# Performance work log

Hardware: AMD Instinct MI355X
Metric: run time of the kernel (lower is better)

## Reference

```python
import jax, jax.numpy as jnp
import numpy as np

C = 256; G = 8; GC = C // G; K = 3; PAD = 1; DIL = 1; STRIDE = 1
P = K * K
BN_EPS = 1e-5; LN_EPS = 1e-5


def setup_inputs() -> dict:
    key = jax.random.key(0)
    ks = jax.random.split(key, 8)
    def rn(k, shape, scale=0.02):
        return jax.random.normal(k, shape, jnp.float32) * scale
    B, H, W = 8, 56, 56
    return dict(
        x=jax.random.normal(ks[0], (B, C, H, W), jnp.float32),
        w_in=rn(ks[1], (C, C)), b_in=jnp.zeros((C,), jnp.float32),
        dw_w=rn(ks[2], (C, 1, K, K)), dw_b=jnp.zeros((C,), jnp.float32),
        ln_g=jnp.ones((C,), jnp.float32), ln_b=jnp.zeros((C,), jnp.float32),
        w_off=rn(ks[3], (C, G * P * 2)), b_off=jnp.zeros((G * P * 2,), jnp.float32),
        w_mask=rn(ks[4], (C, G * P)), b_mask=jnp.zeros((G * P,), jnp.float32),
        w_out=rn(ks[5], (C, C)), b_out=jnp.zeros((C,), jnp.float32),
        bn_g=jnp.ones((C,), jnp.float32), bn_b=jnp.zeros((C,), jnp.float32),
        bn_mean=jnp.zeros((C,), jnp.float32),
        bn_var=jnp.ones((C,), jnp.float32),
    )


def _forward(x, w_in, b_in, dw_w, dw_b, ln_g, ln_b, w_off, b_off,
             w_mask, b_mask, w_out, b_out, bn_g, bn_b, bn_mean, bn_var):
    B, _, H, W = x.shape
    x_nhwc = jnp.transpose(x, (0, 2, 3, 1))                    # [B,H,W,C]
    v = x_nhwc @ w_in + b_in                                   # input_proj

    # offset/mask branch: depthwise conv (NCHW) + LayerNorm (channels_last) + GELU
    f = jax.lax.conv_general_dilated(
        x, dw_w, (1, 1), [(PAD, PAD), (PAD, PAD)],
        feature_group_count=C,
        dimension_numbers=('NCHW', 'OIHW', 'NCHW')) + dw_b[None, :, None, None]
    f = jnp.transpose(f, (0, 2, 3, 1))                         # [B,H,W,C]
    mu = f.mean(-1, keepdims=True)
    var = f.var(-1, keepdims=True)
    f = (f - mu) * jax.lax.rsqrt(var + LN_EPS) * ln_g + ln_b
    f = jax.nn.gelu(f, approximate=False)

    offset = (f @ w_off + b_off).reshape(B, H, W, G, P, 2)     # (x, y) pairs
    mask = jax.nn.softmax((f @ w_mask + b_mask).reshape(B, H, W, G, P), axis=-1)

    # zero-pad projected features (dcnv3_core_pytorch pads before sampling)
    vp = jnp.pad(v, ((0, 0), (PAD, PAD), (PAD, PAD), (0, 0)))
    Hin, Win = H + 2 * PAD, W + 2 * PAD

    # reference points + kernel dilation grid, normalized to padded extent
    base = (DIL * (K - 1)) // 2 + 0.5
    ref_y = (base + jnp.arange(H, dtype=jnp.float32) * STRIDE) / Hin   # [H]
    ref_x = (base + jnp.arange(W, dtype=jnp.float32) * STRIDE) / Win   # [W]
    kx = jnp.arange(K, dtype=jnp.float32) * DIL - (DIL * (K - 1)) // 2
    gx, gy = jnp.meshgrid(kx, kx, indexing='ij')               # torch meshgrid order
    grid_x = gx.reshape(-1) / Win                              # [P]
    grid_y = gy.reshape(-1) / Hin

    loc_x = ref_x[None, None, :, None, None] + grid_x[None, None, None, None, :] + offset[..., 0] / Win
    loc_y = ref_y[None, :, None, None, None] + grid_y[None, None, None, None, :] + offset[..., 1] / Hin
    # grid_sample(align_corners=False) pixel coords: p = loc * size - 0.5
    px = loc_x * Win - 0.5                                     # [B,H,W,G,P]
    py = loc_y * Hin - 0.5

    x0 = jnp.floor(px); y0 = jnp.floor(py)
    wx = px - x0; wy = py - y0
    x0i = x0.astype(jnp.int32); y0i = y0.astype(jnp.int32)
    x1i = x0i + 1; y1i = y0i + 1

    def valid(i, lim):
        return ((i >= 0) & (i < lim)).astype(v.dtype)
    vx0, vx1 = valid(x0i, Win), valid(x1i, Win)
    vy0, vy1 = valid(y0i, Hin), valid(y1i, Hin)
    x0c = jnp.clip(x0i, 0, Win - 1); x1c = jnp.clip(x1i, 0, Win - 1)
    y0c = jnp.clip(y0i, 0, Hin - 1); y1c = jnp.clip(y1i, 0, Hin - 1)

    vg = vp.reshape(B, Hin * Win, G, GC).transpose(0, 2, 1, 3).reshape(B * G, Hin * Win, GC)
    L = H * W

    def regroup(a):  # [B,H,W,G,P] -> [B*G, L*P]
        return a.reshape(B, L, G, P).transpose(0, 2, 1, 3).reshape(B * G, L * P)

    def gather(yc, xc):
        idx = regroup(yc * Win + xc)
        return jnp.take_along_axis(vg, idx[:, :, None], axis=1)   # [B*G, L*P, GC]

    sampled = (gather(y0c, x0c) * regroup((1 - wx) * (1 - wy) * vx0 * vy0)[:, :, None]
             + gather(y0c, x1c) * regroup(wx * (1 - wy) * vx1 * vy0)[:, :, None]
             + gather(y1c, x0c) * regroup((1 - wx) * wy * vx0 * vy1)[:, :, None]
             + gather(y1c, x1c) * regroup(wx * wy * vx1 * vy1)[:, :, None])

    m = mask.reshape(B, L, G, P).transpose(0, 2, 1, 3)             # [B,G,L,P]
    out = (sampled.reshape(B, G, L, P, GC) * m[..., None]).sum(3)  # [B,G,L,GC]
    out = out.transpose(0, 2, 1, 3).reshape(B, H, W, C)

    out = out @ w_out + b_out                                  # output_proj
    y = jnp.transpose(out, (0, 3, 1, 2))                       # NCHW
    y = (y - bn_mean[None, :, None, None]) * jax.lax.rsqrt(bn_var + BN_EPS)[None, :, None, None] \
        * bn_g[None, :, None, None] + bn_b[None, :, None, None]
    return y * jax.nn.sigmoid(y)                               # SiLU


def reference(x, w_in, b_in, dw_w, dw_b, ln_g, ln_b, w_off, b_off,
              w_mask, b_mask, w_out, b_out, bn_g, bn_b, bn_mean, bn_var):
    return _forward(x, w_in, b_in, dw_w, dw_b, ln_g, ln_b, w_off, b_off,
                    w_mask, b_mask, w_out, b_out, bn_g, bn_b, bn_mean, bn_var)
```

## Files before the change

kernel.cpp:

```cpp
#include <hip/hip_runtime.h>
#include <math.h>

#define BATCH 8
#define CH    256
#define HDIM  56
#define WDIM  56
#define HW    (HDIM*WDIM)
#define MTOT  (BATCH*HW)
#define GRP   8
#define GC    32
#define NP    9
#define NOFF  (GRP*NP*2)
#define NMSK  (GRP*NP)
#define NTOT  (NOFF+NMSK)
#define POSB  4
#define NBLK128 ((MTOT/128)*2)
#define NBLKOUT ((MTOT/64)*2)

typedef float f32x4 __attribute__((ext_vector_type(4)));
typedef short s16x8 __attribute__((ext_vector_type(8)));

__device__ inline void split2(float a, float b, unsigned int& hp, unsigned int& lp)
{
    const unsigned int ua = __float_as_uint(a), ub = __float_as_uint(b);
    hp = (ub & 0xffff0000u) | (ua >> 16);
    const float ha = __uint_as_float(ua & 0xffff0000u);
    const float hb = __uint_as_float(ub & 0xffff0000u);
    const unsigned int la = __float_as_uint(a - ha), lb = __float_as_uint(b - hb);
    lp = (lb & 0xffff0000u) | (la >> 16);
}

__device__ __forceinline__ void gld_lds16(const unsigned short* g, unsigned short* l)
{
    __builtin_amdgcn_global_load_lds(
        (const __attribute__((address_space(1))) unsigned int*)g,
        (__attribute__((address_space(3))) unsigned int*)l, 16, 0, 0);
}

__global__ __launch_bounds__(256)
void xt_split_kernel(const float* __restrict__ x,
                     unsigned short* __restrict__ hi,
                     unsigned short* __restrict__ lo)
{
    __shared__ float lds[64][68];
    const int hw0 = blockIdx.x * 64;
    const int k0  = blockIdx.y * 64;
    const int b   = blockIdx.z;
    const int t = threadIdx.x;
    #pragma unroll
    for (int p = 0; p < 4; ++p) {
        const int kr = (t >> 4) + p * 16;
        const int hc = (t & 15) * 4;
        *(float4*)&lds[kr][hc] =
            *(const float4*)(x + ((size_t)b * CH + k0 + kr) * HW + hw0 + hc);
    }
    __syncthreads();
    const int ml = t >> 2;
    const int kc = (t & 3) * 16;
    unsigned int hbuf[8], lbuf[8];
    #pragma unroll
    for (int j = 0; j < 16; j += 2)
        split2(lds[kc + j][ml], lds[kc + j + 1][ml], hbuf[j >> 1], lbuf[j >> 1]);
    const size_t row = (size_t)(b * HW + hw0 + ml) * CH + k0 + kc;
    *(uint4*)&hi[row]     = *(uint4*)&hbuf[0];
    *(uint4*)&hi[row + 8] = *(uint4*)&hbuf[4];
    *(uint4*)&lo[row]     = *(uint4*)&lbuf[0];
    *(uint4*)&lo[row + 8] = *(uint4*)&lbuf[4];
}

__device__ __forceinline__ void gemm128_body(
    const unsigned short* __restrict__ ahi,
    const unsigned short* __restrict__ alo,
    const unsigned short* __restrict__ whi,
    const unsigned short* __restrict__ wlo,
    unsigned short* sAh, unsigned short* sAl,
    unsigned short* sBh, unsigned short* sBl,
    int m0, int n0g, int t, f32x4 (&acc)[4][4])
{
    const int lane = t & 63, wv4 = t >> 6;
    const int wm = wv4 & 1, wn = wv4 >> 1;
    const int fm = lane & 15, q = lane >> 4;

    int srow[2], sgs[2], slb[2];
    #pragma unroll
    for (int i = 0; i < 2; ++i) {
        const int u = i * 256 + t;
        srow[i] = u >> 2;
        const int ss = u & 3;
        sgs[i] = ss ^ ((srow[i] >> 1) & 3);
        slb[i] = i * 2048 + wv4 * 512;
    }

    for (int kk = 0; kk < 8; ++kk) {
        const int k0 = kk * 32;
        #pragma unroll
        for (int i = 0; i < 2; ++i) {
            const size_t ga = (size_t)(m0 + srow[i]) * CH + k0 + sgs[i] * 8;
            const size_t gb = (size_t)(n0g + srow[i]) * CH + k0 + sgs[i] * 8;
            gld_lds16(ahi + ga, sAh + slb[i]);
            gld_lds16(alo + ga, sAl + slb[i]);
            gld_lds16(whi + gb, sBh + slb[i]);
            gld_lds16(wlo + gb, sBl + slb[i]);
        }
        __syncthreads();

        s16x8 ah[4], al[4], wh[4], wl[4];
        #pragma unroll
        for (int i = 0; i < 4; ++i) {
            const int ar = wm * 64 + i * 16 + fm;
            const int as = (q ^ ((ar >> 1) & 3)) * 8;
            ah[i] = *(const s16x8*)&sAh[ar * 32 + as];
            al[i] = *(const s16x8*)&sAl[ar * 32 + as];
            const int br = wn * 64 + i * 16 + fm;
            const int bs = (q ^ ((br >> 1) & 3)) * 8;
            wh[i] = *(const s16x8*)&sBh[br * 32 + bs];
            wl[i] = *(const s16x8*)&sBl[br * 32 + bs];
        }
        #pragma unroll
        for (int nt = 0; nt < 4; ++nt)
            #pragma unroll
            for (int mt = 0; mt < 4; ++mt) {
                acc[nt][mt] = __builtin_amdgcn_mfma_f32_16x16x32_bf16(wh[nt], ah[mt], acc[nt][mt], 0, 0, 0);
                acc[nt][mt] = __builtin_amdgcn_mfma_f32_16x16x32_bf16(wh[nt], al[mt], acc[nt][mt], 0, 0, 0);
                acc[nt][mt] = __builtin_amdgcn_mfma_f32_16x16x32_bf16(wl[nt], ah[mt], acc[nt][mt], 0, 0, 0);
            }
        __syncthreads();
    }
}

__global__ __launch_bounds__(256)
void gemm128_dual(const unsigned short* __restrict__ ahi1,
                  const unsigned short* __restrict__ alo1,
                  const unsigned short* __restrict__ whi1,
                  const unsigned short* __restrict__ wlo1,
                  const float* __restrict__ bias1,
                  float* __restrict__ out1,
                  const unsigned short* __restrict__ ahi2,
                  const unsigned short* __restrict__ alo2,
                  const unsigned short* __restrict__ whi2,
                  const unsigned short* __restrict__ wlo2,
                  const float* __restrict__ bias2,
                  float* __restrict__ out2)
{
    __shared__ unsigned short sAh[128*32], sAl[128*32], sBh[128*32], sBl[128*32];

    const int half = blockIdx.x >= NBLK128;
    const int lbid = blockIdx.x - (half ? NBLK128 : 0);
    const unsigned short* ahi = half ? ahi2 : ahi1;
    const unsigned short* alo = half ? alo2 : alo1;
    const unsigned short* whi = half ? whi2 : whi1;
    const unsigned short* wlo = half ? wlo2 : wlo1;
    const float* bias = half ? bias2 : bias1;
    float* out = half ? out2 : out1;

    const int sw = (lbid & 7) * (NBLK128 / 8) + (lbid >> 3);
    const int m0 = (sw >> 1) * 128;
    const int n0g = (sw & 1) * 128;
    const int t = threadIdx.x;
    const int lane = t & 63, wv4 = t >> 6;
    const int wm = wv4 & 1, wn = wv4 >> 1;
    const int fm = lane & 15, q = lane >> 4;

    f32x4 acc[4][4];
    const f32x4 zero = {0.0f, 0.0f, 0.0f, 0.0f};
    #pragma unroll
    for (int i = 0; i < 4; ++i)
        #pragma unroll
        for (int j = 0; j < 4; ++j) acc[i][j] = zero;

    gemm128_body(ahi, alo, whi, wlo, sAh, sAl, sBh, sBl, m0, n0g, t, acc);

    #pragma unroll
    for (int nt = 0; nt < 4; ++nt) {
        const int n = n0g + wn*64 + nt*16 + q*4;
        const float4 b4 = *(const float4*)&bias[n];
        #pragma unroll
        for (int mt = 0; mt < 4; ++mt) {
            const int mm = m0 + wm*64 + mt*16 + fm;
            f32x4 o = acc[nt][mt];
            o[0] += b4.x; o[1] += b4.y; o[2] += b4.z; o[3] += b4.w;
            *(f32x4*)&out[(size_t)mm * CH + n] = o;
        }
    }
}

__global__ __launch_bounds__(256)
void gemm_out_64x128(const unsigned short* __restrict__ ahi,
                     const unsigned short* __restrict__ alo,
                     const unsigned short* __restrict__ whi,
                     const unsigned short* __restrict__ wlo,
                     const float* __restrict__ bias,
                     const float* __restrict__ bn_g,
                     const float* __restrict__ bn_b,
                     const float* __restrict__ bn_mean,
                     const float* __restrict__ bn_var,
                     float* __restrict__ y)
{
    __shared__ unsigned short sAh[64*32], sAl[64*32], sBh[128*32], sBl[128*32];

    const int sw = (blockIdx.x & 7) * (NBLKOUT / 8) + (blockIdx.x >> 3);
    const int m0  = (sw >> 1) * 64;
    const int n0g = (sw & 1) * 128;
    const int t = threadIdx.x;
    const int lane = t & 63, wv4 = t >> 6;
    const int wm = wv4 >> 1, wn = wv4 & 1;
    const int fm = lane & 15, q = lane >> 4;

    f32x4 acc[4][2];
    const f32x4 zero = {0.0f, 0.0f, 0.0f, 0.0f};
    #pragma unroll
    for (int i = 0; i < 4; ++i)
        #pragma unroll
        for (int j = 0; j < 2; ++j) acc[i][j] = zero;

    const int arow0 = t >> 2;
    const int asl0  = (t & 3) ^ ((arow0 >> 1) & 3);
    const int albase0 = wv4 * 512;
    int brow[2], bsl[2], blbase[2];
    #pragma unroll
    for (int i = 0; i < 2; ++i) {
        const int u = i * 256 + t;
        brow[i] = u >> 2;
        bsl[i] = (u & 3) ^ ((brow[i] >> 1) & 3);
        blbase[i] = i * 2048 + wv4 * 512;
    }

    for (int kk = 0; kk < 8; ++kk) {
        const int k0 = kk * 32;
        {
            const size_t ga = (size_t)(m0 + arow0) * CH + k0 + asl0 * 8;
            gld_lds16(ahi + ga, sAh + albase0);
            gld_lds16(alo + ga, sAl + albase0);
        }
        #pragma unroll
        for (int i = 0; i < 2; ++i) {
            const size_t gb = (size_t)(n0g + brow[i]) * CH + k0 + bsl[i] * 8;
            gld_lds16(whi + gb, sBh + blbase[i]);
            gld_lds16(wlo + gb, sBl + blbase[i]);
        }
        __syncthreads();

        s16x8 ah[2], al[2], wh[4], wl[4];
        #pragma unroll
        for (int i = 0; i < 2; ++i) {
            const int ar = wm * 32 + i * 16 + fm;
            const int as = (q ^ ((ar >> 1) & 3)) * 8;
            ah[i] = *(const s16x8*)&sAh[ar * 32 + as];
            al[i] = *(const s16x8*)&sAl[ar * 32 + as];
        }
        #pragma unroll
        for (int i = 0; i < 4; ++i) {
            const int br = wn * 64 + i * 16 + fm;
            const int bs = (q ^ ((br >> 1) & 3)) * 8;
            wh[i] = *(const s16x8*)&sBh[br * 32 + bs];
            wl[i] = *(const s16x8*)&sBl[br * 32 + bs];
        }
        #pragma unroll
        for (int nt = 0; nt < 4; ++nt)
            #pragma unroll
            for (int mt = 0; mt < 2; ++mt) {
                acc[nt][mt] = __builtin_amdgcn_mfma_f32_16x16x32_bf16(wh[nt], ah[mt], acc[nt][mt], 0, 0, 0);
                acc[nt][mt] = __builtin_amdgcn_mfma_f32_16x16x32_bf16(wh[nt], al[mt], acc[nt][mt], 0, 0, 0);
                acc[nt][mt] = __builtin_amdgcn_mfma_f32_16x16x32_bf16(wl[nt], ah[mt], acc[nt][mt], 0, 0, 0);
            }
        __syncthreads();
    }

    #pragma unroll
    for (int nt = 0; nt < 4; ++nt) {
        #pragma unroll
        for (int r = 0; r < 4; ++r) {
            const int n = n0g + wn*64 + nt*16 + q*4 + r;
            const float sc = bn_g[n] * rsqrtf(bn_var[n] + 1e-5f);
            const float sb = bn_b[n] - bn_mean[n] * sc;
            const float bs = bias[n];
            #pragma unroll
            for (int mt = 0; mt < 2; ++mt) {
                const int mm = m0 + wm*32 + mt*16 + fm;
                const int bimg = mm / HW, hw = mm % HW;
                float val = (acc[nt][mt][r] + bs) * sc + sb;
                y[(size_t)bimg * CH * HW + (size_t)n * HW + hw] = val / (1.0f + expf(-val));
            }
        }
    }
}

__global__ __launch_bounds__(256)
void gemm_in_mfma(const unsigned short* __restrict__ xhi,
                  const unsigned short* __restrict__ xlo,
                  const unsigned short* __restrict__ whi,
                  const unsigned short* __restrict__ wlo,
                  const float* __restrict__ bias,
                  float* __restrict__ v)
{
    const int m0 = blockIdx.x * 256;
    const int n0 = blockIdx.y * 64;
    const int t = threadIdx.x;
    const int lane = t & 63, wv = t >> 6;
    const int mblk = m0 + wv * 64;
    const int fm = lane & 15;
    const int q  = lane >> 4;

    f32x4 acc[4][4];
    const f32x4 zero = {0.0f, 0.0f, 0.0f, 0.0f};
    #pragma unroll
    for (int i = 0; i < 4; ++i)
        #pragma unroll
        for (int j = 0; j < 4; ++j) acc[i][j] = zero;

    const unsigned short *xrh[4], *xrl[4], *wrh[4], *wrl[4];
    #pragma unroll
    for (int mt = 0; mt < 4; ++mt) {
        xrh[mt] = xhi + (size_t)(mblk + mt*16 + fm) * CH + q * 8;
        xrl[mt] = xlo + (size_t)(mblk + mt*16 + fm) * CH + q * 8;
    }
    #pragma unroll
    for (int nt = 0; nt < 4; ++nt) {
        wrh[nt] = whi + (size_t)(n0 + nt*16 + fm) * CH + q * 8;
        wrl[nt] = wlo + (size_t)(n0 + nt*16 + fm) * CH + q * 8;
    }

    for (int k0 = 0; k0 < CH; k0 += 32) {
        s16x8 wh[4], wl[4], ah[4], al[4];
        #pragma unroll
        for (int nt = 0; nt < 4; ++nt) {
            wh[nt] = *(const s16x8*)(wrh[nt] + k0);
            wl[nt] = *(const s16x8*)(wrl[nt] + k0);
        }
        #pragma unroll
        for (int mt = 0; mt < 4; ++mt) {
            ah[mt] = *(const s16x8*)(xrh[mt] + k0);
            al[mt] = *(const s16x8*)(xrl[mt] + k0);
        }
        #pragma unroll
        for (int nt = 0; nt < 4; ++nt)
            #pragma unroll
            for (int mt = 0; mt < 4; ++mt) {
                acc[nt][mt] = __builtin_amdgcn_mfma_f32_16x16x32_bf16(wh[nt], ah[mt], acc[nt][mt], 0, 0, 0);
                acc[nt][mt] = __builtin_amdgcn_mfma_f32_16x16x32_bf16(wh[nt], al[mt], acc[nt][mt], 0, 0, 0);
                acc[nt][mt] = __builtin_amdgcn_mfma_f32_16x16x32_bf16(wl[nt], ah[mt], acc[nt][mt], 0, 0, 0);
            }
    }

    #pragma unroll
    for (int nt = 0; nt < 4; ++nt) {
        const float4 b4 = *(const float4*)&bias[n0 + nt*16 + q*4];
        #pragma unroll
        for (int mt = 0; mt < 4; ++mt) {
            f32x4 o = acc[nt][mt];
            o[0] += b4.x; o[1] += b4.y; o[2] += b4.z; o[3] += b4.w;
            *(f32x4*)&v[(size_t)(mblk + mt*16 + fm) * CH + n0 + nt*16 + q*4] = o;
        }
    }
}

__global__ __launch_bounds__(256)
void dw_ln_gelu_nhwc_split(const unsigned short* __restrict__ xhi,
                           const unsigned short* __restrict__ xlo,
                           const float* __restrict__ dw_w,
                           const float* __restrict__ dw_b,
                           const float* __restrict__ ln_g,
                           const float* __restrict__ ln_b,
                           unsigned short* __restrict__ fh,
                           unsigned short* __restrict__ fl)
{
    __shared__ float wt[NP][CH];
    __shared__ float lbias[CH], lgam[CH], lbet[CH];

    const int t = threadIdx.x;
    {
        const float* wp = dw_w + t * NP;
        #pragma unroll
        for (int p = 0; p < NP; ++p) wt[p][t] = wp[p];
        lbias[t] = dw_b[t]; lgam[t] = ln_g[t]; lbet[t] = ln_b[t];
    }
    __syncthreads();

    const int nblk = MTOT / POSB;
    const int per  = nblk / 8;
    const int bid  = blockIdx.x;
    const int sw   = (bid & 7) * per + (bid >> 3);
    const int q    = t >> 6, lane = t & 63;
    const int n    = sw * POSB + q;
    const int b    = n / HW;
    const int hw   = n % HW;
    const int h    = hw / WDIM, w = hw % WDIM;
    const int c4   = lane * 4;
    const size_t base = (size_t)b * HW * CH + c4;

    float ax = 0.0f, ay = 0.0f, az = 0.0f, aw = 0.0f;
    #pragma unroll
    for (int p = 0; p < NP; ++p) {
        const int hh = h + p / 3 - 1;
        const int ww = w + p % 3 - 1;
        if ((unsigned)hh >= (unsigned)HDIM || (unsigned)ww >= (unsigned)WDIM)
            continue;
        const size_t idx = base + (size_t)(hh * WDIM + ww) * CH;
        const ushort4 uh = *(const ushort4*)(xhi + idx);
        const ushort4 ul = *(const ushort4*)(xlo + idx);
        const float4 wv = *(const float4*)&wt[p][c4];
        ax = fmaf(__uint_as_float((unsigned)uh.x << 16), wv.x,
             fmaf(__uint_as_float((unsigned)ul.x << 16), wv.x, ax));
        ay = fmaf(__uint_as_float((unsigned)uh.y << 16), wv.y,
             fmaf(__uint_as_float((unsigned)ul.y << 16), wv.y, ay));
        az = fmaf(__uint_as_float((unsigned)uh.z << 16), wv.z,
             fmaf(__uint_as_float((unsigned)ul.z << 16), wv.z, az));
        aw = fmaf(__uint_as_float((unsigned)uh.w << 16), wv.w,
             fmaf(__uint_as_float((unsigned)ul.w << 16), wv.w, aw));
    }
    {
        const float4 b4 = *(const float4*)&lbias[c4];
        ax += b4.x; ay += b4.y; az += b4.z; aw += b4.w;
    }

    float s1 = ax + ay + az + aw;
    float s2 = ax*ax + ay*ay + az*az + aw*aw;
    #pragma unroll
    for (int off = 32; off > 0; off >>= 1) {
        s1 += __shfl_xor(s1, off);
        s2 += __shfl_xor(s2, off);
    }
    const float mean = s1 * (1.0f / 256.0f);
    const float rstd = rsqrtf(s2 * (1.0f / 256.0f) - mean * mean + 1e-5f);

    const float4 g4 = *(const float4*)&lgam[c4];
    const float4 e4 = *(const float4*)&lbet[c4];
    const float x0 = (ax - mean) * rstd * g4.x + e4.x;
    const float x1 = (ay - mean) * rstd * g4.y + e4.y;
    const float x2 = (az - mean) * rstd * g4.z + e4.z;
    const float x3 = (aw - mean) * rstd * g4.w + e4.w;
    const float o0 = 0.5f * x0 * (1.0f + erff(x0 * 0.70710678118654752f));
    const float o1 = 0.5f * x1 * (1.0f + erff(x1 * 0.70710678118654752f));
    const float o2 = 0.5f * x2 * (1.0f + erff(x2 * 0.70710678118654752f));
    const float o3 = 0.5f * x3 * (1.0f + erff(x3 * 0.70710678118654752f));

    unsigned int hp0, lp0, hp1, lp1;
    split2(o0, o1, hp0, lp0);
    split2(o2, o3, hp1, lp1);
    *(uint2*)&fh[(size_t)n * CH + c4] = make_uint2(hp0, hp1);
    *(uint2*)&fl[(size_t)n * CH + c4] = make_uint2(lp0, lp1);
}

__global__ __launch_bounds__(256)
void wt_split_kernel(const float* __restrict__ w,
                     unsigned short* __restrict__ hi,
                     unsigned short* __restrict__ lo)
{
    __shared__ float lds[64][68];
    const int kt = blockIdx.x * 64, nt = blockIdx.y * 64;
    const int t = threadIdx.x;
    #pragma unroll
    for (int p = 0; p < 4; ++p) {
        const int kr = (t >> 4) + p * 16, nc = (t & 15) * 4;
        *(float4*)&lds[kr][nc] = *(const float4*)(w + (size_t)(kt + kr) * CH + nt + nc);
    }
    __syncthreads();
    const int nl = t >> 2, kc = (t & 3) * 16;
    #pragma unroll
    for (int j = 0; j < 16; j += 2) {
        const float f0 = lds[kc + j][nl], f1 = lds[kc + j + 1][nl];
        unsigned int hp, lp;
        split2(f0, f1, hp, lp);
        *(unsigned int*)&hi[(size_t)(nt + nl) * CH + kt + kc + j] = hp;
        *(unsigned int*)&lo[(size_t)(nt + nl) * CH + kt + kc + j] = lp;
    }
}

__global__ __launch_bounds__(256)
void wt2_split_kernel(const float* __restrict__ w_off,
                      const float* __restrict__ w_mask,
                      const float* __restrict__ b_off,
                      const float* __restrict__ b_mask,
                      unsigned short* __restrict__ hi,
                      unsigned short* __restrict__ lo,
                      float* __restrict__ bcat)
{
    const int n = threadIdx.x;
    if (blockIdx.x == 0) {
        bcat[n] = (n < NOFF) ? b_off[n] : ((n < NTOT) ? b_mask[n - NOFF] : 0.0f);
    }
    const int k0 = blockIdx.x * 16;
    #pragma unroll
    for (int j = 0; j < 16; j += 2) {
        const int k = k0 + j;
        float f0 = 0.0f, f1 = 0.0f;
        if (n < NOFF) {
            f0 = w_off[(size_t)k * NOFF + n];
            f1 = w_off[(size_t)(k + 1) * NOFF + n];
        } else if (n < NTOT) {
            f0 = w_mask[(size_t)k * NMSK + (n - NOFF)];
            f1 = w_mask[(size_t)(k + 1) * NMSK + (n - NOFF)];
        }
        unsigned int hp, lp;
        split2(f0, f1, hp, lp);
        *(unsigned int*)&hi[(size_t)n * CH + k] = hp;
        *(unsigned int*)&lo[(size_t)n * CH + k] = lp;
    }
}

__global__ __launch_bounds__(256)
void sample_kernel_omb_split(const float* __restrict__ v,
                             const float* __restrict__ omb,
                             unsigned short* __restrict__ sh,
                             unsigned short* __restrict__ sl)
{
    __shared__ alignas(16) float loff[POSB][NOFF];
    __shared__ alignas(16) float lmsk[POSB][NMSK];
    __shared__ alignas(16) float wtab[POSB][GRP*NP][4];
    __shared__ alignas(16) int   itab[POSB][GRP*NP][4];

    const int nblk = MTOT / POSB;
    const int per  = nblk / 8;
    const int bid  = blockIdx.x;
    const int sw   = (bid % 8) * per + (bid / 8);
    const int n0 = sw * POSB;
    const int t = threadIdx.x;

    if (t < POSB * (NOFF/4)) {
        const int q = t / (NOFF/4), r = t % (NOFF/4);
        *(float4*)&loff[q][r*4] = *(const float4*)&omb[(size_t)(n0+q)*CH + r*4];
    } else if (t < POSB * (NOFF/4) + POSB * (NMSK/4)) {
        const int u = t - POSB * (NOFF/4);
        const int q = u / (NMSK/4), r = u % (NMSK/4);
        *(float4*)&lmsk[q][r*4] = *(const float4*)&omb[(size_t)(n0+q)*CH + NOFF + r*4];
    }
    __syncthreads();

    if (t < POSB * GRP) {
        const int q = t >> 3, g = t & 7;
        float* mm = &lmsk[q][g * NP];
        float mx = -1e30f;
        #pragma unroll
        for (int p = 0; p < NP; ++p) mx = fmaxf(mx, mm[p]);
        float sum = 0.0f;
        #pragma unroll
        for (int p = 0; p < NP; ++p) { const float e = __expf(mm[p] - mx); mm[p] = e; sum += e; }
        const float inv = 1.0f / sum;
        #pragma unroll
        for (int p = 0; p < NP; ++p) mm[p] *= inv;
    }
    __syncthreads();

    for (int u = t; u < POSB * GRP * NP; u += 256) {
        const int q = u / (GRP*NP), j = u % (GRP*NP);
        const int g = j / NP, p = j % NP;
        const int n = n0 + q;
        const int hw = n % HW;
        const int h = hw / WDIM, w = hw % WDIM;
        const float ox = loff[q][g*18 + p*2 + 0];
        const float oy = loff[q][g*18 + p*2 + 1];
        const float m  = lmsk[q][g*NP + p];
        const float px = (float)(w + p/3) + ox;
        const float py = (float)(h + p%3) + oy;
        const float fx = floorf(px), fy = floorf(py);
        const float wx = px - fx, wy = py - fy;
        const int x0 = (int)fx, y0 = (int)fy;
        const int x1 = x0 + 1, y1 = y0 + 1;
        const float vx0 = (x0 >= 1 && x0 < 57) ? 1.0f : 0.0f;
        const float vx1 = (x1 >= 1 && x1 < 57) ? 1.0f : 0.0f;
        const float vy0 = (y0 >= 1 && y0 < 57) ? 1.0f : 0.0f;
        const float vy1 = (y1 >= 1 && y1 < 57) ? 1.0f : 0.0f;
        const int x0c = min(max(x0, 1), 56), x1c = min(max(x1, 1), 56);
        const int y0c = min(max(y0, 1), 56), y1c = min(max(y1, 1), 56);
        wtab[q][j][0] = m * (1.0f-wx) * (1.0f-wy) * vx0 * vy0;
        wtab[q][j][1] = m * wx        * (1.0f-wy) * vx1 * vy0;
        wtab[q][j][2] = m * (1.0f-wx) * wy        * vx0 * vy1;
        wtab[q][j][3] = m * wx        * wy        * vx1 * vy1;
        itab[q][j][0] = ((y0c-1)*WDIM + (x0c-1)) * CH;
        itab[q][j][1] = ((y0c-1)*WDIM + (x1c-1)) * CH;
        itab[q][j][2] = ((y1c-1)*WDIM + (x0c-1)) * CH;
        itab[q][j][3] = ((y1c-1)*WDIM + (x1c-1)) * CH;
    }
    __syncthreads();

    const int q = t >> 6, lane = t & 63;
    const int n = n0 + q;
    const int b = n / HW;
    const int g = lane >> 3;
    const float* vb = v + (size_t)b*HW*CH + lane*4;
    float4 acc = {0.0f, 0.0f, 0.0f, 0.0f};
    #pragma unroll
    for (int p = 0; p < NP; ++p) {
        const int j = g*NP + p;
        const float4 wv = *(const float4*)&wtab[q][j][0];
        const int4  iv = *(const int4*)&itab[q][j][0];
        const float4 c0 = *(const float4*)(vb + iv.x);
        const float4 c1 = *(const float4*)(vb + iv.y);
        const float4 c2 = *(const float4*)(vb + iv.z);
        const float4 c3 = *(const float4*)(vb + iv.w);
        acc.x += wv.x*c0.x + wv.y*c1.x + wv.z*c2.x + wv.w*c3.x;
        acc.y += wv.x*c0.y + wv.y*c1.y + wv.z*c2.y + wv.w*c3.y;
        acc.z += wv.x*c0.z + wv.y*c1.z + wv.z*c2.z + wv.w*c3.z;
        acc.w += wv.x*c0.w + wv.y*c1.w + wv.z*c2.w + wv.w*c3.w;
    }
    unsigned int hp0, lp0, hp1, lp1;
    split2(acc.x, acc.y, hp0, lp0);
    split2(acc.z, acc.w, hp1, lp1);
    *(uint2*)&sh[(size_t)n*CH + lane*4] = make_uint2(hp0, hp1);
    *(uint2*)&sl[(size_t)n*CH + lane*4] = make_uint2(lp0, lp1);
}

__global__ __launch_bounds__(256)
void gemm_out_bf16(const unsigned short* __restrict__ shp,
                   const unsigned short* __restrict__ slp,
                   const unsigned short* __restrict__ whi,
                   const unsigned short* __restrict__ wlo,
                   const float* __restrict__ bias,
                   const float* __restrict__ bn_g,
                   const float* __restrict__ bn_b,
                   const float* __restrict__ bn_mean,
                   const float* __restrict__ bn_var,
                   float* __restrict__ y)
{
    const int m0 = blockIdx.x * 256;
    const int n0 = blockIdx.y * 64;
    const int t = threadIdx.x;
    const int lane = t & 63, wv = t >> 6;
    const int mblk = m0 + wv * 64;
    const int fm = lane & 15;
    const int q  = lane >> 4;

    f32x4 acc[4][4];
    const f32x4 zero = {0.0f, 0.0f, 0.0f, 0.0f};
    #pragma unroll
    for (int i = 0; i < 4; ++i)
        #pragma unroll
        for (int j = 0; j < 4; ++j) acc[i][j] = zero;

    const unsigned short *xrh[4], *xrl[4], *wrh[4], *wrl[4];
    #pragma unroll
    for (int mt = 0; mt < 4; ++mt) {
        xrh[mt] = shp + (size_t)(mblk + mt*16 + fm) * CH + q * 8;
        xrl[mt] = slp + (size_t)(mblk + mt*16 + fm) * CH + q * 8;
    }
    #pragma unroll
    for (int nt = 0; nt < 4; ++nt) {
        wrh[nt] = whi + (size_t)(n0 + nt*16 + fm) * CH + q * 8;
        wrl[nt] = wlo + (size_t)(n0 + nt*16 + fm) * CH + q * 8;
    }

    for (int k0 = 0; k0 < CH; k0 += 32) {
        s16x8 wh[4], wl[4], ah[4], al[4];
        #pragma unroll
        for (int nt = 0; nt < 4; ++nt) {
            wh[nt] = *(const s16x8*)(wrh[nt] + k0);
            wl[nt] = *(const s16x8*)(wrl[nt] + k0);
        }
        #pragma unroll
        for (int mt = 0; mt < 4; ++mt) {
            ah[mt] = *(const s16x8*)(xrh[mt] + k0);
            al[mt] = *(const s16x8*)(xrl[mt] + k0);
        }
        #pragma unroll
        for (int nt = 0; nt < 4; ++nt)
            #pragma unroll
            for (int mt = 0; mt < 4; ++mt) {
                acc[nt][mt] = __builtin_amdgcn_mfma_f32_16x16x32_bf16(wh[nt], ah[mt], acc[nt][mt], 0, 0, 0);
                acc[nt][mt] = __builtin_amdgcn_mfma_f32_16x16x32_bf16(wh[nt], al[mt], acc[nt][mt], 0, 0, 0);
                acc[nt][mt] = __builtin_amdgcn_mfma_f32_16x16x32_bf16(wl[nt], ah[mt], acc[nt][mt], 0, 0, 0);
            }
    }

    #pragma unroll
    for (int nt = 0; nt < 4; ++nt) {
        #pragma unroll
        for (int r = 0; r < 4; ++r) {
            const int n = n0 + nt*16 + q*4 + r;
            const float sc = bn_g[n] * rsqrtf(bn_var[n] + 1e-5f);
            const float sb = bn_b[n] - bn_mean[n] * sc;
            const float bs = bias[n];
            #pragma unroll
            for (int mt = 0; mt < 4; ++mt) {
                const int mm = mblk + mt*16;
                const size_t base = (size_t)(mm / HW) * CH * HW + (mm % HW);
                float val = (acc[nt][mt][r] + bs) * sc + sb;
                y[base + (size_t)n * HW + fm] = val / (1.0f + expf(-val));
            }
        }
    }
}

extern "C" void kernel_launch(void* const* d_in, const int* in_sizes, int n_in,
                              void* d_out, int out_size, void* d_ws, size_t ws_size,
                              hipStream_t stream) {
    const float* x      = (const float*)d_in[0];
    const float* w_in   = (const float*)d_in[1];
    const float* b_in   = (const float*)d_in[2];
    const float* dw_w   = (const float*)d_in[3];
    const float* dw_b   = (const float*)d_in[4];
    const float* ln_g   = (const float*)d_in[5];
    const float* ln_b   = (const float*)d_in[6];
    const float* w_off  = (const float*)d_in[7];
    const float* b_off  = (const float*)d_in[8];
    const float* w_mask = (const float*)d_in[9];
    const float* b_mask = (const float*)d_in[10];
    const float* w_out  = (const float*)d_in[11];
    const float* b_out  = (const float*)d_in[12];
    const float* bn_g   = (const float*)d_in[13];
    const float* bn_b   = (const float*)d_in[14];
    const float* bn_mean= (const float*)d_in[15];
    const float* bn_var = (const float*)d_in[16];
    float* out = (float*)d_out;

    const size_t SZ = (size_t)MTOT * CH;
    const size_t need_new =
        4 * SZ * sizeof(float)
        + 6 * (size_t)CH * CH * sizeof(unsigned short)
        + CH * sizeof(float);

    if (ws_size >= need_new) {
        float* ws = (float*)d_ws;
        float* v    = ws;
        unsigned short* xt_hi = (unsigned short*)(v + SZ);
        unsigned short* xt_lo = xt_hi + SZ;
        unsigned short* fh    = xt_lo + SZ;
        unsigned short* fl    = fh + SZ;
        float* omb  = (float*)(fl + SZ);
        unsigned short* wt_hi  = (unsigned short*)(omb + SZ);
        unsigned short* wt_lo  = wt_hi + CH * CH;
        unsigned short* wt2_hi = wt_lo + CH * CH;
        unsigned short* wt2_lo = wt2_hi + CH * CH;
        unsigned short* wt3_hi = wt2_lo + CH * CH;
        unsigned short* wt3_lo = wt3_hi + CH * CH;
        float* bcat = (float*)(wt3_lo + CH * CH);
        unsigned short* sh = xt_hi;
        unsigned short* sl = xt_lo;

        wt_split_kernel<<<dim3(4, 4), dim3(256), 0, stream>>>(w_out, wt_hi, wt_lo);
        wt_split_kernel<<<dim3(4, 4), dim3(256), 0, stream>>>(w_in, wt3_hi, wt3_lo);
        wt2_split_kernel<<<dim3(16), dim3(256), 0, stream>>>(
            w_off, w_mask, b_off, b_mask, wt2_hi, wt2_lo, bcat);
        xt_split_kernel<<<dim3(HW/64, CH/64, BATCH), dim3(256), 0, stream>>>(x, xt_hi, xt_lo);
        dw_ln_gelu_nhwc_split<<<dim3(MTOT/POSB), dim3(256), 0, stream>>>(
            xt_hi, xt_lo, dw_w, dw_b, ln_g, ln_b, fh, fl);
        gemm128_dual<<<dim3(2 * NBLK128), dim3(256), 0, stream>>>(
            xt_hi, xt_lo, wt3_hi, wt3_lo, b_in, v,
            fh, fl, wt2_hi, wt2_lo, bcat, omb);
        sample_kernel_omb_split<<<dim3(MTOT/POSB), dim3(256), 0, stream>>>(v, omb, sh, sl);
        gemm_out_64x128<<<dim3(NBLKOUT), dim3(256), 0, stream>>>(
            sh, sl, wt_hi, wt_lo, b_out, bn_g, bn_b, bn_mean, bn_var, out);
    } else {
        float* ws = (float*)d_ws;
        float* v    = ws;
        unsigned short* xt_hi = (unsigned short*)(v + SZ);
        unsigned short* xt_lo = xt_hi + SZ;
        unsigned short* fh    = xt_lo + SZ;
        unsigned short* fl    = fh + SZ;
        float* omb  = (float*)(fl + SZ);
        unsigned short* wt_hi  = (unsigned short*)(omb + SZ);
        unsigned short* wt_lo  = wt_hi + CH * CH;
        unsigned short* wt2_hi = wt_lo + CH * CH;
        unsigned short* wt2_lo = wt2_hi + CH * CH;
        unsigned short* wt3_hi = wt2_lo + CH * CH;
        unsigned short* wt3_lo = wt3_hi + CH * CH;
        float* bcat = (float*)(wt3_lo + CH * CH);
        unsigned short* sh = xt_hi;
        unsigned short* sl = xt_lo;

        wt_split_kernel<<<dim3(4, 4), dim3(256), 0, stream>>>(w_out, wt_hi, wt_lo);
        wt_split_kernel<<<dim3(4, 4), dim3(256), 0, stream>>>(w_in, wt3_hi, wt3_lo);
        wt2_split_kernel<<<dim3(16), dim3(256), 0, stream>>>(
            w_off, w_mask, b_off, b_mask, wt2_hi, wt2_lo, bcat);
        xt_split_kernel<<<dim3(HW/64, CH/64, BATCH), dim3(256), 0, stream>>>(x, xt_hi, xt_lo);
        gemm_in_mfma<<<dim3(MTOT/256, CH/64), dim3(256), 0, stream>>>(
            xt_hi, xt_lo, wt3_hi, wt3_lo, b_in, v);
        dw_ln_gelu_nhwc_split<<<dim3(MTOT/POSB), dim3(256), 0, stream>>>(
            xt_hi, xt_lo, dw_w, dw_b, ln_g, ln_b, fh, fl);
        gemm_in_mfma<<<dim3(MTOT/256, CH/64), dim3(256), 0, stream>>>(
            fh, fl, wt2_hi, wt2_lo, bcat, omb);
        sample_kernel_omb_split<<<dim3(MTOT/POSB), dim3(256), 0, stream>>>(v, omb, sh, sl);
        gemm_out_bf16<<<dim3(MTOT/256, CH/64), dim3(256), 0, stream>>>(
            sh, sl, wt_hi, wt_lo, b_out, bn_g, bn_b, bn_mean, bn_var, out);
    }
}
```

Baseline: 232.4 us.

## Merge prep kernels and co-schedule depthwise branch with input projection GEMM

Collapses the four weight/input split launches into one prep kernel dispatched by block index. The depthwise conv+LN+GELU work and the input-projection GEMM now run as block ranges of a single kernel, so the independent branches overlap. The offset/mask GEMM is moved into its own launch. The projection GEMMs also switch from 128x128 to 64x128 tiles. The aim is fewer launches and better overlap, at the cost of smaller tiles with less operand reuse and a shared LDS footprint sized for both block types.

```diff
diff --git a/kernel.cpp b/kernel.cpp
--- a/kernel.cpp
+++ b/kernel.cpp
@@ -14,8 +14,9 @@
 #define NMSK  (GRP*NP)
 #define NTOT  (NOFF+NMSK)
 #define POSB  4
-#define NBLK128 ((MTOT/128)*2)
-#define NBLKOUT ((MTOT/64)*2)
+#define DWBLK (MTOT/POSB)
+#define XTBLK (49*4*8)
+#define NBLKG ((MTOT/64)*2)
 
 typedef float f32x4 __attribute__((ext_vector_type(4)));
 typedef short s16x8 __attribute__((ext_vector_type(8)));
@@ -37,80 +38,57 @@
         (__attribute__((address_space(3))) unsigned int*)l, 16, 0, 0);
 }
 
-__global__ __launch_bounds__(256)
-void xt_split_kernel(const float* __restrict__ x,
-                     unsigned short* __restrict__ hi,
-                     unsigned short* __restrict__ lo)
-{
-    __shared__ float lds[64][68];
-    const int hw0 = blockIdx.x * 64;
-    const int k0  = blockIdx.y * 64;
-    const int b   = blockIdx.z;
-    const int t = threadIdx.x;
-    #pragma unroll
-    for (int p = 0; p < 4; ++p) {
-        const int kr = (t >> 4) + p * 16;
-        const int hc = (t & 15) * 4;
-        *(float4*)&lds[kr][hc] =
-            *(const float4*)(x + ((size_t)b * CH + k0 + kr) * HW + hw0 + hc);
-    }
-    __syncthreads();
-    const int ml = t >> 2;
-    const int kc = (t & 3) * 16;
-    unsigned int hbuf[8], lbuf[8];
-    #pragma unroll
-    for (int j = 0; j < 16; j += 2)
-        split2(lds[kc + j][ml], lds[kc + j + 1][ml], hbuf[j >> 1], lbuf[j >> 1]);
-    const size_t row = (size_t)(b * HW + hw0 + ml) * CH + k0 + kc;
-    *(uint4*)&hi[row]     = *(uint4*)&hbuf[0];
-    *(uint4*)&hi[row + 8] = *(uint4*)&hbuf[4];
-    *(uint4*)&lo[row]     = *(uint4*)&lbuf[0];
-    *(uint4*)&lo[row + 8] = *(uint4*)&lbuf[4];
-}
-
-__device__ __forceinline__ void gemm128_body(
+__device__ __forceinline__ void gemm64x128_body(
     const unsigned short* __restrict__ ahi,
     const unsigned short* __restrict__ alo,
     const unsigned short* __restrict__ whi,
     const unsigned short* __restrict__ wlo,
     unsigned short* sAh, unsigned short* sAl,
     unsigned short* sBh, unsigned short* sBl,
-    int m0, int n0g, int t, f32x4 (&acc)[4][4])
+    int m0, int n0g, int t, f32x4 (&acc)[4][2])
 {
     const int lane = t & 63, wv4 = t >> 6;
-    const int wm = wv4 & 1, wn = wv4 >> 1;
+    const int wm = wv4 >> 1;
+    const int wn = wv4 & 1;
     const int fm = lane & 15, q = lane >> 4;
 
-    int srow[2], sgs[2], slb[2];
+    const int arow0 = t >> 2;
+    const int asl0  = (t & 3) ^ ((arow0 >> 1) & 3);
+    const int albase0 = wv4 * 512;
+    int brow[2], bsl[2], blbase[2];
     #pragma unroll
     for (int i = 0; i < 2; ++i) {
         const int u = i * 256 + t;
-        srow[i] = u >> 2;
-        const int ss = u & 3;
-        sgs[i] = ss ^ ((srow[i] >> 1) & 3);
-        slb[i] = i * 2048 + wv4 * 512;
+        brow[i] = u >> 2;
+        bsl[i] = (u & 3) ^ ((brow[i] >> 1) & 3);
+        blbase[i] = i * 2048 + wv4 * 512;
     }
 
     for (int kk = 0; kk < 8; ++kk) {
         const int k0 = kk * 32;
+        {
+            const size_t ga = (size_t)(m0 + arow0) * CH + k0 + asl0 * 8;
+            gld_lds16(ahi + ga, sAh + albase0);
+            gld_lds16(alo + ga, sAl + albase0);
+        }
         #pragma unroll
         for (int i = 0; i < 2; ++i) {
-            const size_t ga = (size_t)(m0 + srow[i]) * CH + k0 + sgs[i] * 8;
-            const size_t gb = (size_t)(n0g + srow[i]) * CH + k0 + sgs[i] * 8;
-            gld_lds16(ahi + ga, sAh + slb[i]);
-            gld_lds16(alo + ga, sAl + slb[i]);
-            gld_lds16(whi + gb, sBh + slb[i]);
-            gld_lds16(wlo + gb, sBl + slb[i]);
+            const size_t gb = (size_t)(n0g + brow[i]) * CH + k0 + bsl[i] * 8;
+            gld_lds16(whi + gb, sBh + blbase[i]);
+            gld_lds16(wlo + gb, sBl + blbase[i]);
         }
         __syncthreads();
 
-        s16x8 ah[4], al[4], wh[4], wl[4];
-        #pragma unroll
-        for (int i = 0; i < 4; ++i) {
-            const int ar = wm * 64 + i * 16 + fm;
+        s16x8 ah[2], al[2], wh[4], wl[4];
+        #pragma unroll
+        for (int i = 0; i < 2; ++i) {
+            const int ar = wm * 32 + i * 16 + fm;
             const int as = (q ^ ((ar >> 1) & 3)) * 8;
             ah[i] = *(const s16x8*)&sAh[ar * 32 + as];
             al[i] = *(const s16x8*)&sAl[ar * 32 + as];
+        }
+        #pragma unroll
+        for (int i = 0; i < 4; ++i) {
             const int br = wn * 64 + i * 16 + fm;
             const int bs = (q ^ ((br >> 1) & 3)) * 8;
             wh[i] = *(const s16x8*)&sBh[br * 32 + bs];
@@ -119,7 +97,7 @@
         #pragma unroll
         for (int nt = 0; nt < 4; ++nt)
             #pragma unroll
-            for (int mt = 0; mt < 4; ++mt) {
+            for (int mt = 0; mt < 2; ++mt) {
                 acc[nt][mt] = __builtin_amdgcn_mfma_f32_16x16x32_bf16(wh[nt], ah[mt], acc[nt][mt], 0, 0, 0);
                 acc[nt][mt] = __builtin_amdgcn_mfma_f32_16x16x32_bf16(wh[nt], al[mt], acc[nt][mt], 0, 0, 0);
                 acc[nt][mt] = __builtin_amdgcn_mfma_f32_16x16x32_bf16(wl[nt], ah[mt], acc[nt][mt], 0, 0, 0);
@@ -128,58 +106,281 @@
     }
 }
 
-__global__ __launch_bounds__(256)
-void gemm128_dual(const unsigned short* __restrict__ ahi1,
-                  const unsigned short* __restrict__ alo1,
-                  const unsigned short* __restrict__ whi1,
-                  const unsigned short* __restrict__ wlo1,
-                  const float* __restrict__ bias1,
-                  float* __restrict__ out1,
-                  const unsigned short* __restrict__ ahi2,
-                  const unsigned short* __restrict__ alo2,
-                  const unsigned short* __restrict__ whi2,
-                  const unsigned short* __restrict__ wlo2,
-                  const float* __restrict__ bias2,
-                  float* __restrict__ out2)
-{
-    __shared__ unsigned short sAh[128*32], sAl[128*32], sBh[128*32], sBl[128*32];
-
-    const int half = blockIdx.x >= NBLK128;
-    const int lbid = blockIdx.x - (half ? NBLK128 : 0);
-    const unsigned short* ahi = half ? ahi2 : ahi1;
-    const unsigned short* alo = half ? alo2 : alo1;
-    const unsigned short* whi = half ? whi2 : whi1;
-    const unsigned short* wlo = half ? wlo2 : wlo1;
-    const float* bias = half ? bias2 : bias1;
-    float* out = half ? out2 : out1;
-
-    const int sw = (lbid & 7) * (NBLK128 / 8) + (lbid >> 3);
-    const int m0 = (sw >> 1) * 128;
+__device__ __forceinline__ void dw_body(
+    const unsigned short* __restrict__ xhi,
+    const unsigned short* __restrict__ xlo,
+    const float* __restrict__ dw_w,
+    const float* __restrict__ dw_b,
+    const float* __restrict__ ln_g,
+    const float* __restrict__ ln_b,
+    unsigned short* __restrict__ fh,
+    unsigned short* __restrict__ fl,
+    float* wt, float* lbias, float* lgam, float* lbet,
+    int bid, int t)
+{
+    {
+        const float* wp = dw_w + t * NP;
+        #pragma unroll
+        for (int p = 0; p < NP; ++p) wt[p * CH + t] = wp[p];
+        lbias[t] = dw_b[t]; lgam[t] = ln_g[t]; lbet[t] = ln_b[t];
+    }
+    __syncthreads();
+
+    const int per = DWBLK / 8;
+    const int sw  = (bid & 7) * per + (bid >> 3);
+    const int q   = t >> 6, lane = t & 63;
+    const int n   = sw * POSB + q;
+    const int b   = n / HW;
+    const int hw  = n % HW;
+    const int h   = hw / WDIM, w = hw % WDIM;
+    const int c4  = lane * 4;
+    const size_t base = (size_t)b * HW * CH + c4;
+
+    float ax = 0.0f, ay = 0.0f, az = 0.0f, aw = 0.0f;
+    #pragma unroll
+    for (int p = 0; p < NP; ++p) {
+        const int hh = h + p / 3 - 1;
+        const int ww = w + p % 3 - 1;
+        if ((unsigned)hh >= (unsigned)HDIM || (unsigned)ww >= (unsigned)WDIM)
+            continue;
+        const size_t idx = base + (size_t)(hh * WDIM + ww) * CH;
+        const ushort4 uh = *(const ushort4*)(xhi + idx);
+        const ushort4 ul = *(const ushort4*)(xlo + idx);
+        const float4 wv = *(const float4*)&wt[p * CH + c4];
+        ax = fmaf(__uint_as_float((unsigned)uh.x << 16), wv.x,
+             fmaf(__uint_as_float((unsigned)ul.x << 16), wv.x, ax));
+        ay = fmaf(__uint_as_float((unsigned)uh.y << 16), wv.y,
+             fmaf(__uint_as_float((unsigned)ul.y << 16), wv.y, ay));
+        az = fmaf(__uint_as_float((unsigned)uh.z << 16), wv.z,
+             fmaf(__uint_as_float((unsigned)ul.z << 16), wv.z, az));
+        aw = fmaf(__uint_as_float((unsigned)uh.w << 16), wv.w,
+             fmaf(__uint_as_float((unsigned)ul.w << 16), wv.w, aw));
+    }
+    {
+        const float4 b4 = *(const float4*)&lbias[c4];
+        ax += b4.x; ay += b4.y; az += b4.z; aw += b4.w;
+    }
+
+    float s1 = ax + ay + az + aw;
+    float s2 = ax*ax + ay*ay + az*az + aw*aw;
+    #pragma unroll
+    for (int off = 32; off > 0; off >>= 1) {
+        s1 += __shfl_xor(s1, off);
+        s2 += __shfl_xor(s2, off);
+    }
+    const float mean = s1 * (1.0f / 256.0f);
+    const float rstd = rsqrtf(s2 * (1.0f / 256.0f) - mean * mean + 1e-5f);
+
+    const float4 g4 = *(const float4*)&lgam[c4];
+    const float4 e4 = *(const float4*)&lbet[c4];
+    const float x0 = (ax - mean) * rstd * g4.x + e4.x;
+    const float x1 = (ay - mean) * rstd * g4.y + e4.y;
+    const float x2 = (az - mean) * rstd * g4.z + e4.z;
+    const float x3 = (aw - mean) * rstd * g4.w + e4.w;
+    const float o0 = 0.5f * x0 * (1.0f + erff(x0 * 0.70710678118654752f));
+    const float o1 = 0.5f * x1 * (1.0f + erff(x1 * 0.70710678118654752f));
+    const float o2 = 0.5f * x2 * (1.0f + erff(x2 * 0.70710678118654752f));
+    const float o3 = 0.5f * x3 * (1.0f + erff(x3 * 0.70710678118654752f));
+
+    unsigned int hp0, lp0, hp1, lp1;
+    split2(o0, o1, hp0, lp0);
+    split2(o2, o3, hp1, lp1);
+    *(uint2*)&fh[(size_t)n * CH + c4] = make_uint2(hp0, hp1);
+    *(uint2*)&fl[(size_t)n * CH + c4] = make_uint2(lp0, lp1);
+}
+
+__global__ __launch_bounds__(256)
+void prep_kernel(const float* __restrict__ x,
+                 unsigned short* __restrict__ xt_hi,
+                 unsigned short* __restrict__ xt_lo,
+                 const float* __restrict__ w_out,
+                 unsigned short* __restrict__ wt_hi,
+                 unsigned short* __restrict__ wt_lo,
+                 const float* __restrict__ w_in,
+                 unsigned short* __restrict__ wt3_hi,
+                 unsigned short* __restrict__ wt3_lo,
+                 const float* __restrict__ w_off,
+                 const float* __restrict__ w_mask,
+                 const float* __restrict__ b_off,
+                 const float* __restrict__ b_mask,
+                 unsigned short* __restrict__ wt2_hi,
+                 unsigned short* __restrict__ wt2_lo,
+                 float* __restrict__ bcat)
+{
+    __shared__ float lds[64][68];
+    const int bid = blockIdx.x;
+    const int t = threadIdx.x;
+
+    if (bid < XTBLK) {
+        const int hw0 = (bid % 49) * 64;
+        const int k0  = ((bid / 49) % 4) * 64;
+        const int b   = bid / 196;
+        #pragma unroll
+        for (int p = 0; p < 4; ++p) {
+            const int kr = (t >> 4) + p * 16;
+            const int hc = (t & 15) * 4;
+            *(float4*)&lds[kr][hc] =
+                *(const float4*)(x + ((size_t)b * CH + k0 + kr) * HW + hw0 + hc);
+        }
+        __syncthreads();
+        const int ml = t >> 2;
+        const int kc = (t & 3) * 16;
+        unsigned int hbuf[8], lbuf[8];
+        #pragma unroll
+        for (int j = 0; j < 16; j += 2)
+            split2(lds[kc + j][ml], lds[kc + j + 1][ml], hbuf[j >> 1], lbuf[j >> 1]);
+        const size_t row = (size_t)(b * HW + hw0 + ml) * CH + k0 + kc;
+        *(uint4*)&xt_hi[row]     = *(uint4*)&hbuf[0];
+        *(uint4*)&xt_hi[row + 8] = *(uint4*)&hbuf[4];
+        *(uint4*)&xt_lo[row]     = *(uint4*)&lbuf[0];
+        *(uint4*)&xt_lo[row + 8] = *(uint4*)&lbuf[4];
+    } else if (bid < XTBLK + 32) {
+        const int u = bid - XTBLK;
+        const float* w = (u < 16) ? w_out : w_in;
+        unsigned short* hi = (u < 16) ? wt_hi : wt3_hi;
+        unsigned short* lo = (u < 16) ? wt_lo : wt3_lo;
+        const int uu = u & 15;
+        const int kt = (uu & 3) * 64, nt = (uu >> 2) * 64;
+        #pragma unroll
+        for (int p = 0; p < 4; ++p) {
+            const int kr = (t >> 4) + p * 16, nc = (t & 15) * 4;
+            *(float4*)&lds[kr][nc] = *(const float4*)(w + (size_t)(kt + kr) * CH + nt + nc);
+        }
+        __syncthreads();
+        const int nl = t >> 2, kc = (t & 3) * 16;
+        #pragma unroll
+        for (int j = 0; j < 16; j += 2) {
+            const float f0 = lds[kc + j][nl], f1 = lds[kc + j + 1][nl];
+            unsigned int hp, lp;
+            split2(f0, f1, hp, lp);
+            *(unsigned int*)&hi[(size_t)(nt + nl) * CH + kt + kc + j] = hp;
+            *(unsigned int*)&lo[(size_t)(nt + nl) * CH + kt + kc + j] = lp;
+        }
+    } else {
+        const int u = bid - XTBLK - 32;
+        const int n = t;
+        if (u == 0) {
+            bcat[n] = (n < NOFF) ? b_off[n] : ((n < NTOT) ? b_mask[n - NOFF] : 0.0f);
+        }
+        const int k0 = u * 16;
+        #pragma unroll
+        for (int j = 0; j < 16; j += 2) {
+            const int k = k0 + j;
+            float f0 = 0.0f, f1 = 0.0f;
+            if (n < NOFF) {
+                f0 = w_off[(size_t)k * NOFF + n];
+                f1 = w_off[(size_t)(k + 1) * NOFF + n];
+            } else if (n < NTOT) {
+                f0 = w_mask[(size_t)k * NMSK + (n - NOFF)];
+                f1 = w_mask[(size_t)(k + 1) * NMSK + (n - NOFF)];
+            }
+            unsigned int hp, lp;
+            split2(f0, f1, hp, lp);
+            *(unsigned int*)&wt2_hi[(size_t)n * CH + k] = hp;
+            *(unsigned int*)&wt2_lo[(size_t)n * CH + k] = lp;
+        }
+    }
+}
+
+__global__ __launch_bounds__(256)
+void dw_and_gemm_v(const unsigned short* __restrict__ xhi,
+                   const unsigned short* __restrict__ xlo,
+                   const float* __restrict__ dw_w,
+                   const float* __restrict__ dw_b,
+                   const float* __restrict__ ln_g,
+                   const float* __restrict__ ln_b,
+                   unsigned short* __restrict__ fh,
+                   unsigned short* __restrict__ fl,
+                   const unsigned short* __restrict__ whi,
+                   const unsigned short* __restrict__ wlo,
+                   const float* __restrict__ bias,
+                   float* __restrict__ v)
+{
+    __shared__ alignas(16) char smem[24576];
+    const int bid = blockIdx.x;
+    const int t = threadIdx.x;
+
+    if (bid < DWBLK) {
+        float* wt    = (float*)smem;
+        float* lbias = (float*)(smem + NP * CH * 4);
+        float* lgam  = lbias + CH;
+        float* lbet  = lgam + CH;
+        dw_body(xhi, xlo, dw_w, dw_b, ln_g, ln_b, fh, fl,
+                wt, lbias, lgam, lbet, bid, t);
+    } else {
+        unsigned short* sAh = (unsigned short*)smem;
+        unsigned short* sAl = sAh + 64 * 32;
+        unsigned short* sBh = sAl + 64 * 32;
+        unsigned short* sBl = sBh + 128 * 32;
+        const int lbid = bid - DWBLK;
+        const int sw = (lbid & 7) * (NBLKG / 8) + (lbid >> 3);
+        const int m0  = (sw >> 1) * 64;
+        const int n0g = (sw & 1) * 128;
+        const int lane = t & 63, wv4 = t >> 6;
+        const int wm = wv4 >> 1, wn = wv4 & 1;
+        const int fm = lane & 15, q = lane >> 4;
+
+        f32x4 acc[4][2];
+        const f32x4 zero = {0.0f, 0.0f, 0.0f, 0.0f};
+        #pragma unroll
+        for (int i = 0; i < 4; ++i)
+            #pragma unroll
+            for (int j = 0; j < 2; ++j) acc[i][j] = zero;
+
+        gemm64x128_body(xhi, xlo, whi, wlo, sAh, sAl, sBh, sBl, m0, n0g, t, acc);
+
+        #pragma unroll
+        for (int nt = 0; nt < 4; ++nt) {
+            const int n = n0g + wn*64 + nt*16 + q*4;
+            const float4 b4 = *(const float4*)&bias[n];
+            #pragma unroll
+            for (int mt = 0; mt < 2; ++mt) {
+                const int mm = m0 + wm*32 + mt*16 + fm;
+                f32x4 o = acc[nt][mt];
+                o[0] += b4.x; o[1] += b4.y; o[2] += b4.z; o[3] += b4.w;
+                *(f32x4*)&v[(size_t)mm * CH + n] = o;
+            }
+        }
+    }
+}
+
+__global__ __launch_bounds__(256)
+void gemm_omb(const unsigned short* __restrict__ ahi,
+              const unsigned short* __restrict__ alo,
+              const unsigned short* __restrict__ whi,
+              const unsigned short* __restrict__ wlo,
+              const float* __restrict__ bias,
+              float* __restrict__ omb)
+{
+    __shared__ unsigned short sAh[64*32], sAl[64*32], sBh[128*32], sBl[128*32];
+
+    const int sw = (blockIdx.x & 7) * (NBLKG / 8) + (blockIdx.x >> 3);
+    const int m0  = (sw >> 1) * 64;
     const int n0g = (sw & 1) * 128;
     const int t = threadIdx.x;
     const int lane = t & 63, wv4 = t >> 6;
-    const int wm = wv4 & 1, wn = wv4 >> 1;
+    const int wm = wv4 >> 1, wn = wv4 & 1;
     const int fm = lane & 15, q = lane >> 4;
 
-    f32x4 acc[4][4];
+    f32x4 acc[4][2];
     const f32x4 zero = {0.0f, 0.0f, 0.0f, 0.0f};
     #pragma unroll
     for (int i = 0; i < 4; ++i)
         #pragma unroll
-        for (int j = 0; j < 4; ++j) acc[i][j] = zero;
-
-    gemm128_body(ahi, alo, whi, wlo, sAh, sAl, sBh, sBl, m0, n0g, t, acc);
+        for (int j = 0; j < 2; ++j) acc[i][j] = zero;
+
+    gemm64x128_body(ahi, alo, whi, wlo, sAh, sAl, sBh, sBl, m0, n0g, t, acc);
 
     #pragma unroll
     for (int nt = 0; nt < 4; ++nt) {
         const int n = n0g + wn*64 + nt*16 + q*4;
         const float4 b4 = *(const float4*)&bias[n];
         #pragma unroll
-        for (int mt = 0; mt < 4; ++mt) {
-            const int mm = m0 + wm*64 + mt*16 + fm;
+        for (int mt = 0; mt < 2; ++mt) {
+            const int mm = m0 + wm*32 + mt*16 + fm;
             f32x4 o = acc[nt][mt];
             o[0] += b4.x; o[1] += b4.y; o[2] += b4.z; o[3] += b4.w;
-            *(f32x4*)&out[(size_t)mm * CH + n] = o;
+            *(f32x4*)&omb[(size_t)mm * CH + n] = o;
         }
     }
 }
@@ -198,7 +399,7 @@
 {
     __shared__ unsigned short sAh[64*32], sAl[64*32], sBh[128*32], sBl[128*32];
 
-    const int sw = (blockIdx.x & 7) * (NBLKOUT / 8) + (blockIdx.x >> 3);
+    const int sw = (blockIdx.x & 7) * (NBLKG / 8) + (blockIdx.x >> 3);
     const int m0  = (sw >> 1) * 64;
     const int n0g = (sw & 1) * 128;
     const int t = threadIdx.x;
@@ -213,58 +414,7 @@
         #pragma unroll
         for (int j = 0; j < 2; ++j) acc[i][j] = zero;
 
-    const int arow0 = t >> 2;
-    const int asl0  = (t & 3) ^ ((arow0 >> 1) & 3);
-    const int albase0 = wv4 * 512;
-    int brow[2], bsl[2], blbase[2];
-    #pragma unroll
-    for (int i = 0; i < 2; ++i) {
-        const int u = i * 256 + t;
-        brow[i] = u >> 2;
-        bsl[i] = (u & 3) ^ ((brow[i] >> 1) & 3);
-        blbase[i] = i * 2048 + wv4 * 512;
-    }
-
-    for (int kk = 0; kk < 8; ++kk) {
-        const int k0 = kk * 32;
-        {
-            const size_t ga = (size_t)(m0 + arow0) * CH + k0 + asl0 * 8;
-            gld_lds16(ahi + ga, sAh + albase0);
-            gld_lds16(alo + ga, sAl + albase0);
-        }
-        #pragma unroll
-        for (int i = 0; i < 2; ++i) {
-            const size_t gb = (size_t)(n0g + brow[i]) * CH + k0 + bsl[i] * 8;
-            gld_lds16(whi + gb, sBh + blbase[i]);
-            gld_lds16(wlo + gb, sBl + blbase[i]);
-        }
-        __syncthreads();
-
-        s16x8 ah[2], al[2], wh[4], wl[4];
-        #pragma unroll
-        for (int i = 0; i < 2; ++i) {
-            const int ar = wm * 32 + i * 16 + fm;
-            const int as = (q ^ ((ar >> 1) & 3)) * 8;
-            ah[i] = *(const s16x8*)&sAh[ar * 32 + as];
-            al[i] = *(const s16x8*)&sAl[ar * 32 + as];
-        }
-        #pragma unroll
-        for (int i = 0; i < 4; ++i) {
-            const int br = wn * 64 + i * 16 + fm;
-            const int bs = (q ^ ((br >> 1) & 3)) * 8;
-            wh[i] = *(const s16x8*)&sBh[br * 32 + bs];
-            wl[i] = *(const s16x8*)&sBl[br * 32 + bs];
-        }
-        #pragma unroll
-        for (int nt = 0; nt < 4; ++nt)
-            #pragma unroll
-            for (int mt = 0; mt < 2; ++mt) {
-                acc[nt][mt] = __builtin_amdgcn_mfma_f32_16x16x32_bf16(wh[nt], ah[mt], acc[nt][mt], 0, 0, 0);
-                acc[nt][mt] = __builtin_amdgcn_mfma_f32_16x16x32_bf16(wh[nt], al[mt], acc[nt][mt], 0, 0, 0);
-                acc[nt][mt] = __builtin_amdgcn_mfma_f32_16x16x32_bf16(wl[nt], ah[mt], acc[nt][mt], 0, 0, 0);
-            }
-        __syncthreads();
-    }
+    gemm64x128_body(ahi, alo, whi, wlo, sAh, sAl, sBh, sBl, m0, n0g, t, acc);
 
     #pragma unroll
     for (int nt = 0; nt < 4; ++nt) {
@@ -286,219 +436,6 @@
 }
 
 __global__ __launch_bounds__(256)
-void gemm_in_mfma(const unsigned short* __restrict__ xhi,
-                  const unsigned short* __restrict__ xlo,
-                  const unsigned short* __restrict__ whi,
-                  const unsigned short* __restrict__ wlo,
-                  const float* __restrict__ bias,
-                  float* __restrict__ v)
-{
-    const int m0 = blockIdx.x * 256;
-    const int n0 = blockIdx.y * 64;
-    const int t = threadIdx.x;
-    const int lane = t & 63, wv = t >> 6;
-    const int mblk = m0 + wv * 64;
-    const int fm = lane & 15;
-    const int q  = lane >> 4;
-
-    f32x4 acc[4][4];
-    const f32x4 zero = {0.0f, 0.0f, 0.0f, 0.0f};
-    #pragma unroll
-    for (int i = 0; i < 4; ++i)
-        #pragma unroll
-        for (int j = 0; j < 4; ++j) acc[i][j] = zero;
-
-    const unsigned short *xrh[4], *xrl[4], *wrh[4], *wrl[4];
-    #pragma unroll
-    for (int mt = 0; mt < 4; ++mt) {
-        xrh[mt] = xhi + (size_t)(mblk + mt*16 + fm) * CH + q * 8;
-        xrl[mt] = xlo + (size_t)(mblk + mt*16 + fm) * CH + q * 8;
-    }
-    #pragma unroll
-    for (int nt = 0; nt < 4; ++nt) {
-        wrh[nt] = whi + (size_t)(n0 + nt*16 + fm) * CH + q * 8;
-        wrl[nt] = wlo + (size_t)(n0 + nt*16 + fm) * CH + q * 8;
-    }
-
-    for (int k0 = 0; k0 < CH; k0 += 32) {
-        s16x8 wh[4], wl[4], ah[4], al[4];
-        #pragma unroll
-        for (int nt = 0; nt < 4; ++nt) {
-            wh[nt] = *(const s16x8*)(wrh[nt] + k0);
-            wl[nt] = *(const s16x8*)(wrl[nt] + k0);
-        }
-        #pragma unroll
-        for (int mt = 0; mt < 4; ++mt) {
-            ah[mt] = *(const s16x8*)(xrh[mt] + k0);
-            al[mt] = *(const s16x8*)(xrl[mt] + k0);
-        }
-        #pragma unroll
-        for (int nt = 0; nt < 4; ++nt)
-            #pragma unroll
-            for (int mt = 0; mt < 4; ++mt) {
-                acc[nt][mt] = __builtin_amdgcn_mfma_f32_16x16x32_bf16(wh[nt], ah[mt], acc[nt][mt], 0, 0, 0);
-                acc[nt][mt] = __builtin_amdgcn_mfma_f32_16x16x32_bf16(wh[nt], al[mt], acc[nt][mt], 0, 0, 0);
-                acc[nt][mt] = __builtin_amdgcn_mfma_f32_16x16x32_bf16(wl[nt], ah[mt], acc[nt][mt], 0, 0, 0);
-            }
-    }
-
-    #pragma unroll
-    for (int nt = 0; nt < 4; ++nt) {
-        const float4 b4 = *(const float4*)&bias[n0 + nt*16 + q*4];
-        #pragma unroll
-        for (int mt = 0; mt < 4; ++mt) {
-            f32x4 o = acc[nt][mt];
-            o[0] += b4.x; o[1] += b4.y; o[2] += b4.z; o[3] += b4.w;
-            *(f32x4*)&v[(size_t)(mblk + mt*16 + fm) * CH + n0 + nt*16 + q*4] = o;
-        }
-    }
-}
-
-__global__ __launch_bounds__(256)
-void dw_ln_gelu_nhwc_split(const unsigned short* __restrict__ xhi,
-                           const unsigned short* __restrict__ xlo,
-                           const float* __restrict__ dw_w,
-                           const float* __restrict__ dw_b,
-                           const float* __restrict__ ln_g,
-                           const float* __restrict__ ln_b,
-                           unsigned short* __restrict__ fh,
-                           unsigned short* __restrict__ fl)
-{
-    __shared__ float wt[NP][CH];
-    __shared__ float lbias[CH], lgam[CH], lbet[CH];
-
-    const int t = threadIdx.x;
-    {
-        const float* wp = dw_w + t * NP;
-        #pragma unroll
-        for (int p = 0; p < NP; ++p) wt[p][t] = wp[p];
-        lbias[t] = dw_b[t]; lgam[t] = ln_g[t]; lbet[t] = ln_b[t];
-    }
-    __syncthreads();
-
-    const int nblk = MTOT / POSB;
-    const int per  = nblk / 8;
-    const int bid  = blockIdx.x;
-    const int sw   = (bid & 7) * per + (bid >> 3);
-    const int q    = t >> 6, lane = t & 63;
-    const int n    = sw * POSB + q;
-    const int b    = n / HW;
-    const int hw   = n % HW;
-    const int h    = hw / WDIM, w = hw % WDIM;
-    const int c4   = lane * 4;
-    const size_t base = (size_t)b * HW * CH + c4;
-
-    float ax = 0.0f, ay = 0.0f, az = 0.0f, aw = 0.0f;
-    #pragma unroll
-    for (int p = 0; p < NP; ++p) {
-        const int hh = h + p / 3 - 1;
-        const int ww = w + p % 3 - 1;
-        if ((unsigned)hh >= (unsigned)HDIM || (unsigned)ww >= (unsigned)WDIM)
-            continue;
-        const size_t idx = base + (size_t)(hh * WDIM + ww) * CH;
-        const ushort4 uh = *(const ushort4*)(xhi + idx);
-        const ushort4 ul = *(const ushort4*)(xlo + idx);
-        const float4 wv = *(const float4*)&wt[p][c4];
-        ax = fmaf(__uint_as_float((unsigned)uh.x << 16), wv.x,
-             fmaf(__uint_as_float((unsigned)ul.x << 16), wv.x, ax));
-        ay = fmaf(__uint_as_float((unsigned)uh.y << 16), wv.y,
-             fmaf(__uint_as_float((unsigned)ul.y << 16), wv.y, ay));
-        az = fmaf(__uint_as_float((unsigned)uh.z << 16), wv.z,
-             fmaf(__uint_as_float((unsigned)ul.z << 16), wv.z, az));
-        aw = fmaf(__uint_as_float((unsigned)uh.w << 16), wv.w,
-             fmaf(__uint_as_float((unsigned)ul.w << 16), wv.w, aw));
-    }
-    {
-        const float4 b4 = *(const float4*)&lbias[c4];
-        ax += b4.x; ay += b4.y; az += b4.z; aw += b4.w;
-    }
-
-    float s1 = ax + ay + az + aw;
-    float s2 = ax*ax + ay*ay + az*az + aw*aw;
-    #pragma unroll
-    for (int off = 32; off > 0; off >>= 1) {
-        s1 += __shfl_xor(s1, off);
-        s2 += __shfl_xor(s2, off);
-    }
-    const float mean = s1 * (1.0f / 256.0f);
-    const float rstd = rsqrtf(s2 * (1.0f / 256.0f) - mean * mean + 1e-5f);
-
-    const float4 g4 = *(const float4*)&lgam[c4];
-    const float4 e4 = *(const float4*)&lbet[c4];
-    const float x0 = (ax - mean) * rstd * g4.x + e4.x;
-    const float x1 = (ay - mean) * rstd * g4.y + e4.y;
-    const float x2 = (az - mean) * rstd * g4.z + e4.z;
-    const float x3 = (aw - mean) * rstd * g4.w + e4.w;
-    const float o0 = 0.5f * x0 * (1.0f + erff(x0 * 0.70710678118654752f));
-    const float o1 = 0.5f * x1 * (1.0f + erff(x1 * 0.70710678118654752f));
-    const float o2 = 0.5f * x2 * (1.0f + erff(x2 * 0.70710678118654752f));
-    const float o3 = 0.5f * x3 * (1.0f + erff(x3 * 0.70710678118654752f));
-
-    unsigned int hp0, lp0, hp1, lp1;
-    split2(o0, o1, hp0, lp0);
-    split2(o2, o3, hp1, lp1);
-    *(uint2*)&fh[(size_t)n * CH + c4] = make_uint2(hp0, hp1);
-    *(uint2*)&fl[(size_t)n * CH + c4] = make_uint2(lp0, lp1);
-}
-
-__global__ __launch_bounds__(256)
-void wt_split_kernel(const float* __restrict__ w,
-                     unsigned short* __restrict__ hi,
-                     unsigned short* __restrict__ lo)
-{
-    __shared__ float lds[64][68];
-    const int kt = blockIdx.x * 64, nt = blockIdx.y * 64;
-    const int t = threadIdx.x;
-    #pragma unroll
-    for (int p = 0; p < 4; ++p) {
-        const int kr = (t >> 4) + p * 16, nc = (t & 15) * 4;
-        *(float4*)&lds[kr][nc] = *(const float4*)(w + (size_t)(kt + kr) * CH + nt + nc);
-    }
-    __syncthreads();
-    const int nl = t >> 2, kc = (t & 3) * 16;
-    #pragma unroll
-    for (int j = 0; j < 16; j += 2) {
-        const float f0 = lds[kc + j][nl], f1 = lds[kc + j + 1][nl];
-        unsigned int hp, lp;
-        split2(f0, f1, hp, lp);
-        *(unsigned int*)&hi[(size_t)(nt + nl) * CH + kt + kc + j] = hp;
-        *(unsigned int*)&lo[(size_t)(nt + nl) * CH + kt + kc + j] = lp;
-    }
-}
-
-__global__ __launch_bounds__(256)
-void wt2_split_kernel(const float* __restrict__ w_off,
-                      const float* __restrict__ w_mask,
-                      const float* __restrict__ b_off,
-                      const float* __restrict__ b_mask,
-                      unsigned short* __restrict__ hi,
-                      unsigned short* __restrict__ lo,
-                      float* __restrict__ bcat)
-{
-    const int n = threadIdx.x;
-    if (blockIdx.x == 0) {
-        bcat[n] = (n < NOFF) ? b_off[n] : ((n < NTOT) ? b_mask[n - NOFF] : 0.0f);
-    }
-    const int k0 = blockIdx.x * 16;
-    #pragma unroll
-    for (int j = 0; j < 16; j += 2) {
-        const int k = k0 + j;
-        float f0 = 0.0f, f1 = 0.0f;
-        if (n < NOFF) {
-            f0 = w_off[(size_t)k * NOFF + n];
-            f1 = w_off[(size_t)(k + 1) * NOFF + n];
-        } else if (n < NTOT) {
-            f0 = w_mask[(size_t)k * NMSK + (n - NOFF)];
-            f1 = w_mask[(size_t)(k + 1) * NMSK + (n - NOFF)];
-        }
-        unsigned int hp, lp;
-        split2(f0, f1, hp, lp);
-        *(unsigned int*)&hi[(size_t)n * CH + k] = hp;
-        *(unsigned int*)&lo[(size_t)n * CH + k] = lp;
-    }
-}
-
-__global__ __launch_bounds__(256)
 void sample_kernel_omb_split(const float* __restrict__ v,
                              const float* __restrict__ omb,
                              unsigned short* __restrict__ sh,
@@ -509,8 +446,7 @@
     __shared__ alignas(16) float wtab[POSB][GRP*NP][4];
     __shared__ alignas(16) int   itab[POSB][GRP*NP][4];
 
-    const int nblk = MTOT / POSB;
-    const int per  = nblk / 8;
+    const int per  = DWBLK / 8;
     const int bid  = blockIdx.x;
     const int sw   = (bid % 8) * per + (bid / 8);
     const int n0 = sw * POSB;
@@ -601,6 +537,245 @@
 }
 
 __global__ __launch_bounds__(256)
+void xt_split_kernel(const float* __restrict__ x,
+                     unsigned short* __restrict__ hi,
+                     unsigned short* __restrict__ lo)
+{
+    __shared__ float lds[64][68];
+    const int hw0 = blockIdx.x * 64;
+    const int k0  = blockIdx.y * 64;
+    const int b   = blockIdx.z;
+    const int t = threadIdx.x;
+    #pragma unroll
+    for (int p = 0; p < 4; ++p) {
+        const int kr = (t >> 4) + p * 16;
+        const int hc = (t & 15) * 4;
+        *(float4*)&lds[kr][hc] =
+            *(const float4*)(x + ((size_t)b * CH + k0 + kr) * HW + hw0 + hc);
+    }
+    __syncthreads();
+    const int ml = t >> 2;
+    const int kc = (t & 3) * 16;
+    unsigned int hbuf[8], lbuf[8];
+    #pragma unroll
+    for (int j = 0; j < 16; j += 2)
+        split2(lds[kc + j][ml], lds[kc + j + 1][ml], hbuf[j >> 1], lbuf[j >> 1]);
+    const size_t row = (size_t)(b * HW + hw0 + ml) * CH + k0 + kc;
+    *(uint4*)&hi[row]     = *(uint4*)&hbuf[0];
+    *(uint4*)&hi[row + 8] = *(uint4*)&hbuf[4];
+    *(uint4*)&lo[row]     = *(uint4*)&lbuf[0];
+    *(uint4*)&lo[row + 8] = *(uint4*)&lbuf[4];
+}
+
+__global__ __launch_bounds__(256)
+void wt_split_kernel(const float* __restrict__ w,
+                     unsigned short* __restrict__ hi,
+                     unsigned short* __restrict__ lo)
+{
+    __shared__ float lds[64][68];
+    const int kt = blockIdx.x * 64, nt = blockIdx.y * 64;
+    const int t = threadIdx.x;
+    #pragma unroll
+    for (int p = 0; p < 4; ++p) {
+        const int kr = (t >> 4) + p * 16, nc = (t & 15) * 4;
+        *(float4*)&lds[kr][nc] = *(const float4*)(w + (size_t)(kt + kr) * CH + nt + nc);
+    }
+    __syncthreads();
+    const int nl = t >> 2, kc = (t & 3) * 16;
+    #pragma unroll
+    for (int j = 0; j < 16; j += 2) {
+        const float f0 = lds[kc + j][nl], f1 = lds[kc + j + 1][nl];
+        unsigned int hp, lp;
+        split2(f0, f1, hp, lp);
+        *(unsigned int*)&hi[(size_t)(nt + nl) * CH + kt + kc + j] = hp;
+        *(unsigned int*)&lo[(size_t)(nt + nl) * CH + kt + kc + j] = lp;
+    }
+}
+
+__global__ __launch_bounds__(256)
+void wt2_split_kernel(const float* __restrict__ w_off,
+                      const float* __restrict__ w_mask,
+                      const float* __restrict__ b_off,
+                      const float* __restrict__ b_mask,
+                      unsigned short* __restrict__ hi,
+                      unsigned short* __restrict__ lo,
+                      float* __restrict__ bcat)
+{
+    const int n = threadIdx.x;
+    if (blockIdx.x == 0) {
+        bcat[n] = (n < NOFF) ? b_off[n] : ((n < NTOT) ? b_mask[n - NOFF] : 0.0f);
+    }
+    const int k0 = blockIdx.x * 16;
+    #pragma unroll
+    for (int j = 0; j < 16; j += 2) {
+        const int k = k0 + j;
+        float f0 = 0.0f, f1 = 0.0f;
+        if (n < NOFF) {
+            f0 = w_off[(size_t)k * NOFF + n];
+            f1 = w_off[(size_t)(k + 1) * NOFF + n];
+        } else if (n < NTOT) {
+            f0 = w_mask[(size_t)k * NMSK + (n - NOFF)];
+            f1 = w_mask[(size_t)(k + 1) * NMSK + (n - NOFF)];
+        }
+        unsigned int hp, lp;
+        split2(f0, f1, hp, lp);
+        *(unsigned int*)&hi[(size_t)n * CH + k] = hp;
+        *(unsigned int*)&lo[(size_t)n * CH + k] = lp;
+    }
+}
+
+__global__ __launch_bounds__(256)
+void gemm_in_mfma(const unsigned short* __restrict__ xhi,
+                  const unsigned short* __restrict__ xlo,
+                  const unsigned short* __restrict__ whi,
+                  const unsigned short* __restrict__ wlo,
+                  const float* __restrict__ bias,
+                  float* __restrict__ v)
+{
+    const int m0 = blockIdx.x * 256;
+    const int n0 = blockIdx.y * 64;
+    const int t = threadIdx.x;
+    const int lane = t & 63, wv = t >> 6;
+    const int mblk = m0 + wv * 64;
+    const int fm = lane & 15;
+    const int q  = lane >> 4;
+
+    f32x4 acc[4][4];
+    const f32x4 zero = {0.0f, 0.0f, 0.0f, 0.0f};
+    #pragma unroll
+    for (int i = 0; i < 4; ++i)
+        #pragma unroll
+        for (int j = 0; j < 4; ++j) acc[i][j] = zero;
+
+    const unsigned short *xrh[4], *xrl[4], *wrh[4], *wrl[4];
+    #pragma unroll
+    for (int mt = 0; mt < 4; ++mt) {
+        xrh[mt] = xhi + (size_t)(mblk + mt*16 + fm) * CH + q * 8;
+        xrl[mt] = xlo + (size_t)(mblk + mt*16 + fm) * CH + q * 8;
+    }
+    #pragma unroll
+    for (int nt = 0; nt < 4; ++nt) {
+        wrh[nt] = whi + (size_t)(n0 + nt*16 + fm) * CH + q * 8;
+        wrl[nt] = wlo + (size_t)(n0 + nt*16 + fm) * CH + q * 8;
+    }
+
+    for (int k0 = 0; k0 < CH; k0 += 32) {
+        s16x8 wh[4], wl[4], ah[4], al[4];
+        #pragma unroll
+        for (int nt = 0; nt < 4; ++nt) {
+            wh[nt] = *(const s16x8*)(wrh[nt] + k0);
+            wl[nt] = *(const s16x8*)(wrl[nt] + k0);
+        }
+        #pragma unroll
+        for (int mt = 0; mt < 4; ++mt) {
+            ah[mt] = *(const s16x8*)(xrh[mt] + k0);
+            al[mt] = *(const s16x8*)(xrl[mt] + k0);
+        }
+        #pragma unroll
+        for (int nt = 0; nt < 4; ++nt)
+            #pragma unroll
+            for (int mt = 0; mt < 4; ++mt) {
+                acc[nt][mt] = __builtin_amdgcn_mfma_f32_16x16x32_bf16(wh[nt], ah[mt], acc[nt][mt], 0, 0, 0);
+                acc[nt][mt] = __builtin_amdgcn_mfma_f32_16x16x32_bf16(wh[nt], al[mt], acc[nt][mt], 0, 0, 0);
+                acc[nt][mt] = __builtin_amdgcn_mfma_f32_16x16x32_bf16(wl[nt], ah[mt], acc[nt][mt], 0, 0, 0);
+            }
+    }
+
+    #pragma unroll
+    for (int nt = 0; nt < 4; ++nt) {
+        const float4 b4 = *(const float4*)&bias[n0 + nt*16 + q*4];
+        #pragma unroll
+        for (int mt = 0; mt < 4; ++mt) {
+            f32x4 o = acc[nt][mt];
+            o[0] += b4.x; o[1] += b4.y; o[2] += b4.z; o[3] += b4.w;
+            *(f32x4*)&v[(size_t)(mblk + mt*16 + fm) * CH + n0 + nt*16 + q*4] = o;
+        }
+    }
+}
+
+__global__ __launch_bounds__(256)
+void dw_ln_gelu_nhwc_split(const unsigned short* __restrict__ xhi,
+                           const unsigned short* __restrict__ xlo,
+                           const float* __restrict__ dw_w,
+                           const float* __restrict__ dw_b,
+                           const float* __restrict__ ln_g,
+                           const float* __restrict__ ln_b,
+                           unsigned short* __restrict__ fh,
+                           unsigned short* __restrict__ fl)
+{
+    __shared__ float wt[NP][CH];
+    __shared__ float lbias[CH], lgam[CH], lbet[CH];
+    const int t = threadIdx.x;
+    {
+        const float* wp = dw_w + t * NP;
+        #pragma unroll
+        for (int p = 0; p < NP; ++p) wt[p][t] = wp[p];
+        lbias[t] = dw_b[t]; lgam[t] = ln_g[t]; lbet[t] = ln_b[t];
+    }
+    __syncthreads();
+
+    const int per  = DWBLK / 8;
+    const int bid  = blockIdx.x;
+    const int sw   = (bid & 7) * per + (bid >> 3);
+    const int q    = t >> 6, lane = t & 63;
+    const int n    = sw * POSB + q;
+    const int b    = n / HW;
+    const int hw   = n % HW;
+    const int h    = hw / WDIM, w = hw % WDIM;
+    const int c4   = lane * 4;
+    const size_t base = (size_t)b * HW * CH + c4;
+
+    float ax = 0.0f, ay = 0.0f, az = 0.0f, aw = 0.0f;
+    #pragma unroll
+    for (int p = 0; p < NP; ++p) {
+        const int hh = h + p / 3 - 1;
+        const int ww = w + p % 3 - 1;
+        if ((unsigned)hh >= (unsigned)HDIM || (unsigned)ww >= (unsigned)WDIM)
+            continue;
+        const size_t idx = base + (size_t)(hh * WDIM + ww) * CH;
+        const ushort4 uh = *(const ushort4*)(xhi + idx);
+        const ushort4 ul = *(const ushort4*)(xlo + idx);
+        const float4 wv = *(const float4*)&wt[p][c4];
+        ax = fmaf(__uint_as_float((unsigned)uh.x << 16), wv.x,
+             fmaf(__uint_as_float((unsigned)ul.x << 16), wv.x, ax));
+        ay = fmaf(__uint_as_float((unsigned)uh.y << 16), wv.y,
+             fmaf(__uint_as_float((unsigned)ul.y << 16), wv.y, ay));
+        az = fmaf(__uint_as_float((unsigned)uh.z << 16), wv.z,
+             fmaf(__uint_as_float((unsigned)ul.z << 16), wv.z, az));
+        aw = fmaf(__uint_as_float((unsigned)uh.w << 16), wv.w,
+             fmaf(__uint_as_float((unsigned)ul.w << 16), wv.w, aw));
+    }
+    {
+        const float4 b4 = *(const float4*)&lbias[c4];
+        ax += b4.x; ay += b4.y; az += b4.z; aw += b4.w;
+    }
+    float s1 = ax + ay + az + aw;
+    float s2 = ax*ax + ay*ay + az*az + aw*aw;
+    #pragma unroll
+    for (int off = 32; off > 0; off >>= 1) {
+        s1 += __shfl_xor(s1, off);
+        s2 += __shfl_xor(s2, off);
+    }
+    const float mean = s1 * (1.0f / 256.0f);
+    const float rstd = rsqrtf(s2 * (1.0f / 256.0f) - mean * mean + 1e-5f);
+    const float4 g4 = *(const float4*)&lgam[c4];
+    const float4 e4 = *(const float4*)&lbet[c4];
+    const float x0 = (ax - mean) * rstd * g4.x + e4.x;
+    const float x1 = (ay - mean) * rstd * g4.y + e4.y;
+    const float x2 = (az - mean) * rstd * g4.z + e4.z;
+    const float x3 = (aw - mean) * rstd * g4.w + e4.w;
+    const float o0 = 0.5f * x0 * (1.0f + erff(x0 * 0.70710678118654752f));
+    const float o1 = 0.5f * x1 * (1.0f + erff(x1 * 0.70710678118654752f));
+    const float o2 = 0.5f * x2 * (1.0f + erff(x2 * 0.70710678118654752f));
+    const float o3 = 0.5f * x3 * (1.0f + erff(x3 * 0.70710678118654752f));
+    unsigned int hp0, lp0, hp1, lp1;
+    split2(o0, o1, hp0, lp0);
+    split2(o2, o3, hp1, lp1);
+    *(uint2*)&fh[(size_t)n * CH + c4] = make_uint2(hp0, hp1);
+    *(uint2*)&fl[(size_t)n * CH + c4] = make_uint2(lp0, lp1);
+}
+
+__global__ __launch_bounds__(256)
 void gemm_out_bf16(const unsigned short* __restrict__ shp,
                    const unsigned short* __restrict__ slp,
                    const unsigned short* __restrict__ whi,
@@ -726,18 +901,16 @@
         unsigned short* sh = xt_hi;
         unsigned short* sl = xt_lo;
 
-        wt_split_kernel<<<dim3(4, 4), dim3(256), 0, stream>>>(w_out, wt_hi, wt_lo);
-        wt_split_kernel<<<dim3(4, 4), dim3(256), 0, stream>>>(w_in, wt3_hi, wt3_lo);
-        wt2_split_kernel<<<dim3(16), dim3(256), 0, stream>>>(
+        prep_kernel<<<dim3(XTBLK + 48), dim3(256), 0, stream>>>(
+            x, xt_hi, xt_lo, w_out, wt_hi, wt_lo, w_in, wt3_hi, wt3_lo,
             w_off, w_mask, b_off, b_mask, wt2_hi, wt2_lo, bcat);
-        xt_split_kernel<<<dim3(HW/64, CH/64, BATCH), dim3(256), 0, stream>>>(x, xt_hi, xt_lo);
-        dw_ln_gelu_nhwc_split<<<dim3(MTOT/POSB), dim3(256), 0, stream>>>(
-            xt_hi, xt_lo, dw_w, dw_b, ln_g, ln_b, fh, fl);
-        gemm128_dual<<<dim3(2 * NBLK128), dim3(256), 0, stream>>>(
-            xt_hi, xt_lo, wt3_hi, wt3_lo, b_in, v,
+        dw_and_gemm_v<<<dim3(DWBLK + NBLKG), dim3(256), 0, stream>>>(
+            xt_hi, xt_lo, dw_w, dw_b, ln_g, ln_b, fh, fl,
+            wt3_hi, wt3_lo, b_in, v);
+        gemm_omb<<<dim3(NBLKG), dim3(256), 0, stream>>>(
             fh, fl, wt2_hi, wt2_lo, bcat, omb);
-        sample_kernel_omb_split<<<dim3(MTOT/POSB), dim3(256), 0, stream>>>(v, omb, sh, sl);
-        gemm_out_64x128<<<dim3(NBLKOUT), dim3(256), 0, stream>>>(
+        sample_kernel_omb_split<<<dim3(DWBLK), dim3(256), 0, stream>>>(v, omb, sh, sl);
+        gemm_out_64x128<<<dim3(NBLKG), dim3(256), 0, stream>>>(
             sh, sl, wt_hi, wt_lo, b_out, bn_g, bn_b, bn_mean, bn_var, out);
     } else {
         float* ws = (float*)d_ws;
@@ -764,11 +937,11 @@
         xt_split_kernel<<<dim3(HW/64, CH/64, BATCH), dim3(256), 0, stream>>>(x, xt_hi, xt_lo);
         gemm_in_mfma<<<dim3(MTOT/256, CH/64), dim3(256), 0, stream>>>(
             xt_hi, xt_lo, wt3_hi, wt3_lo, b_in, v);
-        dw_ln_gelu_nhwc_split<<<dim3(MTOT/POSB), dim3(256), 0, stream>>>(
+        dw_ln_gelu_nhwc_split<<<dim3(DWBLK), dim3(256), 0, stream>>>(
             xt_hi, xt_lo, dw_w, dw_b, ln_g, ln_b, fh, fl);
         gemm_in_mfma<<<dim3(MTOT/256, CH/64), dim3(256), 0, stream>>>(
             fh, fl, wt2_hi, wt2_lo, bcat, omb);
-        sample_kernel_omb_split<<<dim3(MTOT/POSB), dim3(256), 0, stream>>>(v, omb, sh, sl);
+        sample_kernel_omb_split<<<dim3(DWBLK), dim3(256), 0, stream>>>(v, omb, sh, sl);
         gemm_out_bf16<<<dim3(MTOT/256, CH/64), dim3(256), 0, stream>>>(
             sh, sl, wt_hi, wt_lo, b_out, bn_g, bn_b, bn_mean, bn_var, out);
     }
```

New measurement: 229.3 us. No clear change (-1.3%).
